# Kernel tuning notes

Hardware: AMD Instinct MI355X
Metric: run time of the kernel (lower is better)

Reference implementation:

```python
import jax, jax.numpy as jnp
import numpy as np

B, F0, D = 2048, 40, 32
LAYER0, LAYER1 = 128, 128  # layer_size=(128,128), split_half=True -> field_nums=[40,64]


def setup_inputs() -> dict:
    key = jax.random.key(0)
    k1, k2, k3 = jax.random.split(key, 3)
    x = jax.random.normal(k1, (B, F0, D), dtype=jnp.float32)
    # TF conv1d filters: [1, F_prev*F0, size]; we store them reshaped [F0, F_prev_fields, size]
    # Layer 0: F_prev = F0 = 40 -> W0 flattened index m = i*F0 + j, i over x0 fields, j over hidden fields
    W0 = jax.random.normal(k2, (F0, F0, LAYER0), dtype=jnp.float32) * 0.05
    b0 = jnp.zeros((LAYER0,), dtype=jnp.float32)
    # Layer 1: F_prev = LAYER0 // 2 = 64 (split_half)
    W1 = jax.random.normal(k3, (F0, LAYER0 // 2, LAYER1), dtype=jnp.float32) * 0.05
    b1 = jnp.zeros((LAYER1,), dtype=jnp.float32)
    return {"x": x, "W0": W0, "b0": b0, "W1": W1, "b1": b1}


def reference(x, W0, b0, W1, b1):
    # CIN layer 0: outer product x0 (x) x0 over fields per embedding dim, then 1x1 conv + bias + relu
    # TF flattens dot_result as index i*F_prev + j, matching W0[i, j, s].
    h0 = jax.nn.relu(jnp.einsum('bid,bjd,ijs->bsd', x, x, W0) + b0[None, :, None])  # (B, 128, D)
    half = LAYER0 // 2
    next_hidden, direct0 = h0[:, :half, :], h0[:, half:, :]  # split_half
    # CIN layer 1 (last layer): all feature maps go to direct connect
    direct1 = jax.nn.relu(
        jnp.einsum('bid,bjd,ijs->bsd', x, next_hidden, W1) + b1[None, :, None]
    )  # (B, 128, D)
    result = jnp.concatenate([direct0, direct1], axis=1)  # (B, 192, D)
    return jnp.sum(result, axis=-1)  # (B, 192)
```

## Files before the change

### kernel.cpp

```cpp
#include <hip/hip_runtime.h>
#include <stdint.h>


typedef __attribute__((ext_vector_type(8))) _Float16 half8;
typedef __attribute__((ext_vector_type(2))) _Float16 half2v;
typedef __attribute__((ext_vector_type(4))) float f32x4;

__device__ __forceinline__ unsigned short f2h(float f) {
    return __builtin_bit_cast(unsigned short, (_Float16)f);
}
__device__ __forceinline__ float qsum(float v) {
    v += __shfl_xor(v, 16, 64);
    v += __shfl_xor(v, 32, 64);
    return v;
}

__global__ void permute_w_both(const float* __restrict__ W0, const float* __restrict__ W1,
                               unsigned short* __restrict__ Wp0, unsigned short* __restrict__ Wp1)
{
    int t = blockIdx.x;
    int s = threadIdx.x >> 1, h = threadIdx.x & 1;
    const float* W; unsigned short* Wp; int JW, tt;
    if (t < 50) { W = W0; Wp = Wp0; JW = 40; tt = t; }
    else        { W = W1; Wp = Wp1; JW = 64; tt = t - 50; }
    int jc = tt / 10, ic = tt - jc * 10;
    unsigned short outv[16];
    #pragma unroll
    for (int q = 0; q < 16; ++q) {
        int kl = h * 16 + q;
        int i = ic * 4 + (kl >> 3), j = jc * 8 + (kl & 7);
        outv[q] = f2h(W[((size_t)(i * JW + j)) * 128 + s]);
    }
    unsigned short* dst = Wp + (size_t)tt * 4096 + s * 32 + h * 16;
    *(uint4*)dst       = *(const uint4*)outv;
    *(uint4*)(dst + 8) = *(const uint4*)(outv + 8);
}

template<int NJC>
__device__ __forceinline__ void gemm_phase_reg(
    const unsigned short* __restrict__ Wp,
    const unsigned short* __restrict__ Jl,
    int jstride,
    const unsigned int xi2[4][10],
    f32x4 acc[4][4], int tid)
{
    const int lane = tid & 63;
    const int mw = (tid >> 6) & 1;
    const int nw = tid >> 7;
    const int ml = lane & 15;
    const int kc = lane >> 4;
    const unsigned short* wt = Wp + ((nw * 64 + ml) * 32 + kc * 8);
    const unsigned short* jrow[4];
    #pragma unroll
    for (int mt = 0; mt < 4; ++mt)
        jrow[mt] = Jl + (mw * 64 + mt * 16 + ml) * jstride;

    uint4 bv[4];
    #pragma unroll
    for (int nt = 0; nt < 4; ++nt) bv[nt] = *(const uint4*)(wt + nt * 512);

    uint4 jv[4], jvn[4];
    #pragma unroll
    for (int mt = 0; mt < 4; ++mt) jv[mt] = *(const uint4*)(jrow[mt]);

    for (int jc = 0; jc < NJC; ++jc) {
        if (jc + 1 < NJC) {
            #pragma unroll
            for (int mt = 0; mt < 4; ++mt) jvn[mt] = *(const uint4*)(jrow[mt] + (jc + 1) * 8);
        } else {
            #pragma unroll
            for (int mt = 0; mt < 4; ++mt) jvn[mt] = jv[mt];
        }
        #pragma unroll
        for (int ic = 0; ic < 10; ++ic) {
            const unsigned short* wn;
            if (ic < 9) wn = wt + 4096;
            else        wn = (jc + 1 < NJC) ? wt + 4096 : wt;
            uint4 bn[4];
            #pragma unroll
            for (int nt = 0; nt < 4; ++nt) bn[nt] = *(const uint4*)(wn + nt * 512);
            uint4 av[4];
            #pragma unroll
            for (int mt = 0; mt < 4; ++mt) {
                half2v x2 = __builtin_bit_cast(half2v, xi2[mt][ic]);
                av[mt].x = __builtin_bit_cast(unsigned int,
                    (half2v)(x2 * __builtin_bit_cast(half2v, jv[mt].x)));
                av[mt].y = __builtin_bit_cast(unsigned int,
                    (half2v)(x2 * __builtin_bit_cast(half2v, jv[mt].y)));
                av[mt].z = __builtin_bit_cast(unsigned int,
                    (half2v)(x2 * __builtin_bit_cast(half2v, jv[mt].z)));
                av[mt].w = __builtin_bit_cast(unsigned int,
                    (half2v)(x2 * __builtin_bit_cast(half2v, jv[mt].w)));
            }
            #pragma unroll
            for (int mt = 0; mt < 4; ++mt)
                #pragma unroll
                for (int nt = 0; nt < 4; ++nt)
                    acc[mt][nt] = __builtin_amdgcn_mfma_f32_16x16x32_f16(
                        __builtin_bit_cast(half8, av[mt]),
                        __builtin_bit_cast(half8, bv[nt]),
                        acc[mt][nt], 0, 0, 0);
            #pragma unroll
            for (int nt = 0; nt < 4; ++nt) bv[nt] = bn[nt];
            wt = wn;
        }
        #pragma unroll
        for (int mt = 0; mt < 4; ++mt) jv[mt] = jvn[mt];
    }
}

__global__ __launch_bounds__(256, 2)
void fused_two_layer(const float* __restrict__ x,
                     const unsigned short* __restrict__ W0p,
                     const float* __restrict__ b0,
                     const unsigned short* __restrict__ W1p,
                     const float* __restrict__ b1,
                     float* __restrict__ out)
{
    __shared__ __align__(16) unsigned short Xl[128 * 40];
    __shared__ __align__(16) unsigned short NH[128 * 72];

    const int tid  = threadIdx.x;
    const int lane = tid & 63;
    const int mw   = (tid >> 6) & 1;
    const int nw   = tid >> 7;
    const int ml   = lane & 15;
    const int kc   = lane >> 4;

    const float* xblk = x + (size_t)blockIdx.x * (4 * 40 * 32);
    #pragma unroll
    for (int bl = 0; bl < 4; ++bl) {
        #pragma unroll
        for (int k = 0; k < 5; ++k) {
            int e = 256 * k + tid;
            int i = e >> 5, d = e & 31;
            Xl[(bl * 32 + d) * 40 + i] = f2h(xblk[bl * 1280 + e]);
        }
    }
    __syncthreads();

    unsigned int xi2[4][10];
    #pragma unroll
    for (int mt = 0; mt < 4; ++mt) {
        const unsigned short* xr = Xl + (mw * 64 + mt * 16 + ml) * 40;
        #pragma unroll
        for (int ic = 0; ic < 10; ++ic) {
            unsigned int u = xr[ic * 4 + kc];
            xi2[mt][ic] = u | (u << 16);
        }
    }

    f32x4 acc[4][4];
    const f32x4 zero4 = {0.f, 0.f, 0.f, 0.f};
    #pragma unroll
    for (int mt = 0; mt < 4; ++mt)
        #pragma unroll
        for (int nt = 0; nt < 4; ++nt) acc[mt][nt] = zero4;

    gemm_phase_reg<5>(W0p, Xl, 40, xi2, acc, tid);

    {
        float bias[4];
        #pragma unroll
        for (int nt = 0; nt < 4; ++nt) bias[nt] = b0[nw * 64 + nt * 16 + ml];
        if (nw == 0) {
            #pragma unroll
            for (int mt = 0; mt < 4; ++mt) {
                int r = mw * 64 + mt * 16 + (kc << 2);
                #pragma unroll
                for (int nt = 0; nt < 4; ++nt) {
                    int s = nt * 16 + ml;
                    #pragma unroll
                    for (int rg = 0; rg < 4; ++rg) {
                        float v = fmaxf(acc[mt][nt][rg] + bias[nt], 0.0f);
                        NH[(r + rg) * 72 + s] = f2h(v);
                    }
                }
            }
        } else {
            int bb = blockIdx.x * 4 + mw * 2;
            #pragma unroll
            for (int nt = 0; nt < 4; ++nt) {
                float sA = 0.f, sB = 0.f;
                #pragma unroll
                for (int rg = 0; rg < 4; ++rg) {
                    sA += fmaxf(acc[0][nt][rg] + bias[nt], 0.f) + fmaxf(acc[1][nt][rg] + bias[nt], 0.f);
                    sB += fmaxf(acc[2][nt][rg] + bias[nt], 0.f) + fmaxf(acc[3][nt][rg] + bias[nt], 0.f);
                }
                sA = qsum(sA); sB = qsum(sB);
                if (lane < 16) {
                    out[(size_t)bb * 192 + nt * 16 + lane]       = sA;
                    out[(size_t)(bb + 1) * 192 + nt * 16 + lane] = sB;
                }
            }
        }
    }
    __syncthreads();

    #pragma unroll
    for (int mt = 0; mt < 4; ++mt)
        #pragma unroll
        for (int nt = 0; nt < 4; ++nt) acc[mt][nt] = zero4;

    gemm_phase_reg<8>(W1p, NH, 72, xi2, acc, tid);

    {
        float bias[4];
        #pragma unroll
        for (int nt = 0; nt < 4; ++nt) bias[nt] = b1[nw * 64 + nt * 16 + ml];
        int bb = blockIdx.x * 4 + mw * 2;
        #pragma unroll
        for (int nt = 0; nt < 4; ++nt) {
            float sA = 0.f, sB = 0.f;
            #pragma unroll
            for (int rg = 0; rg < 4; ++rg) {
                sA += fmaxf(acc[0][nt][rg] + bias[nt], 0.f) + fmaxf(acc[1][nt][rg] + bias[nt], 0.f);
                sB += fmaxf(acc[2][nt][rg] + bias[nt], 0.f) + fmaxf(acc[3][nt][rg] + bias[nt], 0.f);
            }
            sA = qsum(sA); sB = qsum(sB);
            if (lane < 16) {
                out[(size_t)bb * 192 + 64 + nw * 64 + nt * 16 + lane]       = sA;
                out[(size_t)(bb + 1) * 192 + 64 + nw * 64 + nt * 16 + lane] = sB;
            }
        }
    }
}

extern "C" void kernel_launch(void* const* d_in, const int* in_sizes, int n_in,
                              void* d_out, int out_size, void* d_ws, size_t ws_size,
                              hipStream_t stream) {
    const float* x  = (const float*)d_in[0];
    const float* W0 = (const float*)d_in[1];
    const float* b0 = (const float*)d_in[2];
    const float* W1 = (const float*)d_in[3];
    const float* b1 = (const float*)d_in[4];
    float* out = (float*)d_out;

    unsigned short* W0p = (unsigned short*)d_ws;
    unsigned short* W1p = (unsigned short*)((char*)d_ws + 50 * 4096 * 2);

    permute_w_both<<<130, 256, 0, stream>>>(W0, W1, W0p, W1p);
    fused_two_layer<<<512, 256, 0, stream>>>(x, W0p, b0, W1p, b1, out);
}
```

Measured before the change: 129.0 us.

## Stage weight tiles in double-buffered LDS and double batch rows per block

Each block now covers 8 batch items with 512 threads instead of 4 with 256. Weight tiles are cooperatively loaded from global memory into a double-buffered LDS buffer, and each wave reads its B fragments from LDS instead of fetching them per wave from global/L2. The goal is to share weight loads across twice as many rows and cut redundant global traffic. The cost is a __syncthreads every k-step, more LDS per block, and only 256 blocks, which may lower occupancy and leave MFMA issue exposed to barrier stalls.

```diff
diff --git a/kernel.cpp b/kernel.cpp
--- a/kernel.cpp
+++ b/kernel.cpp
@@ -37,31 +37,39 @@
 }
 
 template<int NJC>
-__device__ __forceinline__ void gemm_phase_reg(
+__device__ __forceinline__ void gemm_phase(
     const unsigned short* __restrict__ Wp,
     const unsigned short* __restrict__ Jl,
     int jstride,
     const unsigned int xi2[4][10],
+    unsigned short* Wb,
     f32x4 acc[4][4], int tid)
 {
+    constexpr int T = NJC * 10;
     const int lane = tid & 63;
-    const int mw = (tid >> 6) & 1;
-    const int nw = tid >> 7;
+    const int rt = (tid >> 6) & 3;
+    const int sh = tid >> 8;
     const int ml = lane & 15;
     const int kc = lane >> 4;
-    const unsigned short* wt = Wp + ((nw * 64 + ml) * 32 + kc * 8);
+
     const unsigned short* jrow[4];
     #pragma unroll
     for (int mt = 0; mt < 4; ++mt)
-        jrow[mt] = Jl + (mw * 64 + mt * 16 + ml) * jstride;
-
-    uint4 bv[4];
-    #pragma unroll
-    for (int nt = 0; nt < 4; ++nt) bv[nt] = *(const uint4*)(wt + nt * 512);
-
+        jrow[mt] = Jl + (rt * 64 + mt * 16 + ml) * jstride;
+
+    const unsigned short* brd = Wb + (sh * 64 + ml) * 32 + kc * 8;
+    unsigned short* bwr = Wb + tid * 8;
+
+    uint4 wrn;
+    {
+        uint4 w0 = *(const uint4*)(Wp + tid * 8);
+        *(uint4*)bwr = w0;
+        wrn = *(const uint4*)(Wp + 4096 + tid * 8);
+    }
     uint4 jv[4], jvn[4];
     #pragma unroll
     for (int mt = 0; mt < 4; ++mt) jv[mt] = *(const uint4*)(jrow[mt]);
+    __syncthreads();
 
     for (int jc = 0; jc < NJC; ++jc) {
         if (jc + 1 < NJC) {
@@ -73,12 +81,19 @@
         }
         #pragma unroll
         for (int ic = 0; ic < 10; ++ic) {
-            const unsigned short* wn;
-            if (ic < 9) wn = wt + 4096;
-            else        wn = (jc + 1 < NJC) ? wt + 4096 : wt;
-            uint4 bn[4];
-            #pragma unroll
-            for (int nt = 0; nt < 4; ++nt) bn[nt] = *(const uint4*)(wn + nt * 512);
+            const int tt = jc * 10 + ic;
+            const int cb = ic & 1;
+            const int nb = cb ^ 1;
+            if (tt + 1 < T) *(uint4*)(bwr + nb * 4096) = wrn;
+            {
+                const unsigned short* wg =
+                    Wp + (size_t)((tt + 2 < T) ? (tt + 2) : tt) * 4096 + tid * 8;
+                wrn = *(const uint4*)wg;
+            }
+            uint4 bv[4];
+            #pragma unroll
+            for (int nt = 0; nt < 4; ++nt)
+                bv[nt] = *(const uint4*)(brd + cb * 4096 + nt * 512);
             uint4 av[4];
             #pragma unroll
             for (int mt = 0; mt < 4; ++mt) {
@@ -100,16 +115,14 @@
                         __builtin_bit_cast(half8, av[mt]),
                         __builtin_bit_cast(half8, bv[nt]),
                         acc[mt][nt], 0, 0, 0);
-            #pragma unroll
-            for (int nt = 0; nt < 4; ++nt) bv[nt] = bn[nt];
-            wt = wn;
+            __syncthreads();
         }
         #pragma unroll
         for (int mt = 0; mt < 4; ++mt) jv[mt] = jvn[mt];
     }
 }
 
-__global__ __launch_bounds__(256, 2)
+__global__ __launch_bounds__(512, 2)
 void fused_two_layer(const float* __restrict__ x,
                      const unsigned short* __restrict__ W0p,
                      const float* __restrict__ b0,
@@ -117,24 +130,27 @@
                      const float* __restrict__ b1,
                      float* __restrict__ out)
 {
-    __shared__ __align__(16) unsigned short Xl[128 * 40];
-    __shared__ __align__(16) unsigned short NH[128 * 72];
+    __shared__ __align__(16) unsigned short Xl[256 * 40];
+    __shared__ __align__(16) unsigned short NH[256 * 72];
+    __shared__ __align__(16) unsigned short Wb[2 * 4096];
 
     const int tid  = threadIdx.x;
     const int lane = tid & 63;
-    const int mw   = (tid >> 6) & 1;
-    const int nw   = tid >> 7;
+    const int rt   = (tid >> 6) & 3;
+    const int sh   = tid >> 8;
     const int ml   = lane & 15;
     const int kc   = lane >> 4;
 
-    const float* xblk = x + (size_t)blockIdx.x * (4 * 40 * 32);
-    #pragma unroll
-    for (int bl = 0; bl < 4; ++bl) {
-        #pragma unroll
-        for (int k = 0; k < 5; ++k) {
-            int e = 256 * k + tid;
-            int i = e >> 5, d = e & 31;
-            Xl[(bl * 32 + d) * 40 + i] = f2h(xblk[bl * 1280 + e]);
+    const float* xblk = x + (size_t)blockIdx.x * (8 * 40 * 32);
+    #pragma unroll
+    for (int bl = 0; bl < 8; ++bl) {
+        #pragma unroll
+        for (int k = 0; k < 3; ++k) {
+            int f = 512 * k + tid;
+            if (f < 1280) {
+                int i = f >> 5, d = f & 31;
+                Xl[(bl * 32 + d) * 40 + i] = f2h(xblk[bl * 1280 + f]);
+            }
         }
     }
     __syncthreads();
@@ -142,7 +158,7 @@
     unsigned int xi2[4][10];
     #pragma unroll
     for (int mt = 0; mt < 4; ++mt) {
-        const unsigned short* xr = Xl + (mw * 64 + mt * 16 + ml) * 40;
+        const unsigned short* xr = Xl + (rt * 64 + mt * 16 + ml) * 40;
         #pragma unroll
         for (int ic = 0; ic < 10; ++ic) {
             unsigned int u = xr[ic * 4 + kc];
@@ -157,16 +173,16 @@
         #pragma unroll
         for (int nt = 0; nt < 4; ++nt) acc[mt][nt] = zero4;
 
-    gemm_phase_reg<5>(W0p, Xl, 40, xi2, acc, tid);
+    gemm_phase<5>(W0p, Xl, 40, xi2, Wb, acc, tid);
 
     {
         float bias[4];
         #pragma unroll
-        for (int nt = 0; nt < 4; ++nt) bias[nt] = b0[nw * 64 + nt * 16 + ml];
-        if (nw == 0) {
+        for (int nt = 0; nt < 4; ++nt) bias[nt] = b0[sh * 64 + nt * 16 + ml];
+        if (sh == 0) {
             #pragma unroll
             for (int mt = 0; mt < 4; ++mt) {
-                int r = mw * 64 + mt * 16 + (kc << 2);
+                int r = rt * 64 + mt * 16 + (kc << 2);
                 #pragma unroll
                 for (int nt = 0; nt < 4; ++nt) {
                     int s = nt * 16 + ml;
@@ -178,7 +194,7 @@
                 }
             }
         } else {
-            int bb = blockIdx.x * 4 + mw * 2;
+            int bb = blockIdx.x * 8 + rt * 2;
             #pragma unroll
             for (int nt = 0; nt < 4; ++nt) {
                 float sA = 0.f, sB = 0.f;
@@ -189,8 +205,9 @@
                 }
                 sA = qsum(sA); sB = qsum(sB);
                 if (lane < 16) {
-                    out[(size_t)bb * 192 + nt * 16 + lane]       = sA;
-                    out[(size_t)(bb + 1) * 192 + nt * 16 + lane] = sB;
+                    int col = nt * 16 + lane;
+                    out[(size_t)bb * 192 + col]       = sA;
+                    out[(size_t)(bb + 1) * 192 + col] = sB;
                 }
             }
         }
@@ -202,13 +219,13 @@
         #pragma unroll
         for (int nt = 0; nt < 4; ++nt) acc[mt][nt] = zero4;
 
-    gemm_phase_reg<8>(W1p, NH, 72, xi2, acc, tid);
+    gemm_phase<8>(W1p, NH, 72, xi2, Wb, acc, tid);
 
     {
         float bias[4];
         #pragma unroll
-        for (int nt = 0; nt < 4; ++nt) bias[nt] = b1[nw * 64 + nt * 16 + ml];
-        int bb = blockIdx.x * 4 + mw * 2;
+        for (int nt = 0; nt < 4; ++nt) bias[nt] = b1[sh * 64 + nt * 16 + ml];
+        int bb = blockIdx.x * 8 + rt * 2;
         #pragma unroll
         for (int nt = 0; nt < 4; ++nt) {
             float sA = 0.f, sB = 0.f;
@@ -219,8 +236,9 @@
             }
             sA = qsum(sA); sB = qsum(sB);
             if (lane < 16) {
-                out[(size_t)bb * 192 + 64 + nw * 64 + nt * 16 + lane]       = sA;
-                out[(size_t)(bb + 1) * 192 + 64 + nw * 64 + nt * 16 + lane] = sB;
+                int col = 64 + sh * 64 + nt * 16 + lane;
+                out[(size_t)bb * 192 + col]       = sA;
+                out[(size_t)(bb + 1) * 192 + col] = sB;
             }
         }
     }
@@ -240,5 +258,5 @@
     unsigned short* W1p = (unsigned short*)((char*)d_ws + 50 * 4096 * 2);
 
     permute_w_both<<<130, 256, 0, stream>>>(W0, W1, W0p, W1p);
-    fused_two_layer<<<512, 256, 0, stream>>>(x, W0p, b0, W1p, b1, out);
-}
+    fused_two_layer<<<256, 512, 0, stream>>>(x, W0p, b0, W1p, b1, out);
+}
```

After: 131.3 us. No clear change (+1.9%).
